# Optimization experiments

Hardware: AMD Instinct MI355X
Metric: run time of the kernel (lower is better)

Reference implementation:

```python
import jax, jax.numpy as jnp
import numpy as np

L, D, H, DH, W, G, FF = 2, 768, 12, 64, 256, 64, 3072  # W = one-sided window (attention_window=512)
B, S = 2, 4096
NEG = -1e9


def setup_inputs() -> dict:
    key = jax.random.key(0)
    ks = jax.random.split(key, 16)
    inp = {}
    inp['hidden_states'] = jax.random.normal(ks[0], (B, S, D), jnp.float32)
    # HF Longformer convention: <0 masked, >0 global, 0 local. First G tokens are global.
    inp['attention_mask'] = jnp.zeros((B, S), jnp.float32).at[:, :G].set(1.0)
    inp['padding_len'] = 0
    inp['level_hierarchy'] = 0
    def w(k, shape):
        return (jax.random.normal(k, shape, jnp.float32) * 0.02)
    for i, n in enumerate(['Wq', 'Wk', 'Wv', 'Wqg', 'Wkg', 'Wvg', 'Wo']):
        inp[n] = w(ks[1 + i], (L, D, D))
        inp['b' + n[1:].lower()] = jnp.zeros((L, D), jnp.float32)
    inp['Wi'] = w(ks[8], (L, D, FF)); inp['bi'] = jnp.zeros((L, FF), jnp.float32)
    inp['Wo2'] = w(ks[9], (L, FF, D)); inp['bo2'] = jnp.zeros((L, D), jnp.float32)
    for n in ['ln1', 'ln2']:
        inp[n + '_g'] = jnp.ones((L, D), jnp.float32)
        inp[n + '_b'] = jnp.zeros((L, D), jnp.float32)
    return inp


def _ln(x, g, b):
    mu = jnp.mean(x, -1, keepdims=True)
    var = jnp.mean(jnp.square(x - mu), -1, keepdims=True)
    return (x - mu) * jax.lax.rsqrt(var + 1e-5) * g + b


def _chunk3(x, nc, w):
    # x: [..., S, d] -> [..., nc, 3w, d]: keys of chunks (c-1, c, c+1), zero-padded at the ends
    shp = x.shape
    xr = x.reshape(shp[:-2] + (nc, w, shp[-1]))
    pad = [(0, 0)] * xr.ndim
    pad[-3] = (1, 1)
    xp = jnp.pad(xr, pad)
    return jnp.concatenate([xp[..., :-2, :, :], xp[..., 1:-1, :, :], xp[..., 2:, :, :]], axis=-2)


def _layer(h, mask, Wq, bq, Wk, bk, Wv, bv, Wqg, bqg, Wkg, bkg, Wvg, bvg,
           Wo, bo, ln1_g, ln1_b, Wi, bi, Wo2, bo2, ln2_g, ln2_b):
    Bb, Ss, Dd = h.shape
    nc = Ss // W
    scale = 1.0 / np.sqrt(DH)
    def heads(x):
        return x.reshape(Bb, Ss, H, DH).transpose(0, 2, 1, 3)  # [B,H,S,dh]
    q = heads(h @ Wq + bq) * scale
    k = heads(h @ Wk + bk)
    v = heads(h @ Wv + bv)
    # --- sliding-window (banded) attention, chunked ---
    qc = q.reshape(Bb, H, nc, W, DH)
    k3 = _chunk3(k, nc, W)  # [B,H,nc,3W,dh]
    v3 = _chunk3(v, nc, W)
    local = jnp.einsum('bhcid,bhcjd->bhcij', qc, k3)  # [B,H,nc,W,3W]
    i = jnp.arange(W)[:, None]
    j = jnp.arange(3 * W)[None, :]
    band_ok = jnp.abs(j - W - i) <= W                              # [W,3W]
    keypos = jnp.arange(nc)[:, None, None] * W + (j - W)[None]     # [nc,1,3W]
    in_range = (keypos >= 0) & (keypos < Ss)
    # masked and global keys are removed from the windowed attention (handled via global cols)
    key_local = _chunk3((mask == 0).astype(h.dtype)[..., None], nc, W)[..., 0] > 0.5  # [B,nc,3W]
    valid = band_ok[None, None] & in_range[None] & key_local[:, :, None, :]  # [B,nc,W,3W]
    local = jnp.where(valid[:, None], local, NEG)
    # --- global key columns (every token attends to the G global tokens) ---
    kg, vg = k[:, :, :G], v[:, :, :G]
    sg = jnp.einsum('bhsd,bhgd->bhsg', q, kg).reshape(Bb, H, nc, W, G)
    probs = jax.nn.softmax(jnp.concatenate([sg, local], axis=-1), axis=-1)
    pg, pl = probs[..., :G], probs[..., G:]
    out = (jnp.einsum('bhcig,bhgd->bhcid', pg, vg)
           + jnp.einsum('bhcij,bhcjd->bhcid', pl, v3)).reshape(Bb, H, Ss, DH)
    # --- global token rows: full attention with dedicated global projections ---
    qg = heads(h @ Wqg + bqg)[:, :, :G] * scale
    kgf = heads(h @ Wkg + bkg)
    vgf = heads(h @ Wvg + bvg)
    add = jnp.where(mask < 0, NEG, 0.0)[:, None, None, :]
    pgl = jax.nn.softmax(jnp.einsum('bhgd,bhsd->bhgs', qg, kgf) + add, axis=-1)
    out = out.at[:, :, :G].set(jnp.einsum('bhgs,bhsd->bhgd', pgl, vgf))
    out = jnp.where((mask < 0)[:, None, :, None], 0.0, out)
    attn = out.transpose(0, 2, 1, 3).reshape(Bb, Ss, Dd) @ Wo + bo
    h = _ln(attn + h, ln1_g, ln1_b)
    ff = jax.nn.gelu(h @ Wi + bi, approximate=False) @ Wo2 + bo2
    return _ln(ff + h, ln2_g, ln2_b)


def reference(hidden_states, attention_mask, padding_len, level_hierarchy,
              Wq, bq, Wk, bk, Wv, bv, Wqg, bqg, Wkg, bkg, Wvg, bvg,
              Wo, bo, ln1_g, ln1_b, Wi, bi, Wo2, bo2, ln2_g, ln2_b):
    h = hidden_states
    for l in range(L):
        h = _layer(h, attention_mask,
                   Wq[l], bq[l], Wk[l], bk[l], Wv[l], bv[l],
                   Wqg[l], bqg[l], Wkg[l], bkg[l], Wvg[l], bvg[l],
                   Wo[l], bo[l], ln1_g[l], ln1_b[l],
                   Wi[l], bi[l], Wo2[l], bo2[l], ln2_g[l], ln2_b[l])
    if padding_len > 0:
        h = h[:, :-padding_len]
    return h
```

## Files before the change

### kernel.cpp

```cpp
#include <hip/hip_runtime.h>

#define B_ 2
#define S_ 4096
#define D_ 768
#define H_ 12
#define DH_ 64
#define W_ 256
#define G_ 64
#define FF_ 3072
#define L_ 2
#define M_ (B_*S_)
#define NEGV -1e9f
#define NSPLIT 16

typedef short bf16x8 __attribute__((ext_vector_type(8)));
typedef float f32x4 __attribute__((ext_vector_type(4)));
typedef unsigned short u16;
typedef unsigned short u16x4 __attribute__((ext_vector_type(4)));

__device__ __forceinline__ u16 f2bf(float f) {
  union { float f; unsigned u; } a; a.f = f;
  unsigned r = a.u + 0x7FFFu + ((a.u >> 16) & 1u);
  return (u16)(r >> 16);
}
__device__ __forceinline__ float b2f(u16 u) {
  union { unsigned u; float f; } a; a.u = ((unsigned)u) << 16;
  return a.f;
}

__device__ __forceinline__ f32x4 mfma16(bf16x8 a, bf16x8 b, f32x4 c) {
  return __builtin_amdgcn_mfma_f32_16x16x32_bf16(a, b, c, 0, 0, 0);
}

__device__ __forceinline__ void gload16(const u16* g, u16* l) {
  __builtin_amdgcn_global_load_lds((const __attribute__((address_space(1))) void*)g,
                                   (__attribute__((address_space(3))) void*)l, 16, 0, 0);
}

__device__ __forceinline__ int xcd_swz(int bid, int nwg) {
  if ((nwg & 7) == 0) {
    int cpx = nwg >> 3;
    bid = (bid & 7) * cpx + (bid >> 3);
  }
  return bid;
}

struct Ptr7 { const float* p[7]; };
__global__ __launch_bounds__(256) void wtrans7(Ptr7 in, u16* __restrict__ out) {
  __shared__ float tile[32][33];
  int z = blockIdx.z;
  int slab = z >> 1, l = z & 1;
  const float* src = in.p[slab] + (size_t)l * D_ * D_;
  u16* dst = out + (size_t)z * D_ * D_;
  int k0 = blockIdx.y * 32, n0 = blockIdx.x * 32;
  int tx = threadIdx.x, ty = threadIdx.y;
#pragma unroll
  for (int i = 0; i < 4; i++)
    tile[ty + i*8][tx] = src[(size_t)(k0 + ty + i*8) * D_ + n0 + tx];
  __syncthreads();
#pragma unroll
  for (int i = 0; i < 4; i++)
    dst[(size_t)(n0 + ty + i*8) * D_ + k0 + tx] = f2bf(tile[tx][ty + i*8]);
}

__global__ __launch_bounds__(256) void wtrans(const float* __restrict__ in,
                                              u16* __restrict__ out, int K, int N) {
  __shared__ float tile[32][33];
  size_t base = (size_t)blockIdx.z * K * N;
  int k0 = blockIdx.y * 32, n0 = blockIdx.x * 32;
  int tx = threadIdx.x, ty = threadIdx.y;
#pragma unroll
  for (int i = 0; i < 4; i++)
    tile[ty + i*8][tx] = in[base + (size_t)(k0 + ty + i*8) * N + n0 + tx];
  __syncthreads();
#pragma unroll
  for (int i = 0; i < 4; i++)
    out[base + (size_t)(n0 + ty + i*8) * K + k0 + tx] = f2bf(tile[tx][ty + i*8]);
}

__global__ __launch_bounds__(256) void conv_b(const float* __restrict__ in,
                                              u16* __restrict__ outb, int n4) {
  int i = blockIdx.x * 256 + threadIdx.x;
  if (i >= n4) return;
  float4 v = ((const float4*)in)[i];
  u16x4 o;
  o[0] = f2bf(v.x); o[1] = f2bf(v.y); o[2] = f2bf(v.z); o[3] = f2bf(v.w);
  ((u16x4*)outb)[i] = o;
}

template <int MODE>
__device__ __forceinline__ float epi_post(float v) {
  if (MODE == 2) return v * 0.125f;
  if (MODE == 3) {
    float y = 0.79788456f * (v + 0.044715f * v * v * v);
    float e = __expf(fminf(2.f * y, 20.f));
    return v * e / (e + 1.f);
  }
  return v;
}

struct Bias5 { const float* p[5]; };

#define VMC4() asm volatile("s_waitcnt vmcnt(4)" ::: "memory")
#define VMC0() asm volatile("s_waitcnt vmcnt(0)" ::: "memory")
#define GPH_PRE() do { __builtin_amdgcn_s_barrier(); \
  asm volatile("s_waitcnt lgkmcnt(0)" ::: "memory"); \
  __builtin_amdgcn_sched_barrier(0); } while (0)
#define GPH_PRE_NOLDS() do { __builtin_amdgcn_s_barrier(); \
  __builtin_amdgcn_sched_barrier(0); } while (0)
#define GPH_POST() do { __builtin_amdgcn_sched_barrier(0); \
  __builtin_amdgcn_s_barrier(); } while (0)
#define GPH_MFMA(AF, BF, QM, QN) do { \
  __builtin_amdgcn_s_setprio(1); \
  _Pragma("unroll") for (int mi = 0; mi < 4; mi++) \
  _Pragma("unroll") for (int nj = 0; nj < 2; nj++) \
  _Pragma("unroll") for (int ks = 0; ks < 2; ks++) \
    acc[(QM)*4+mi][(QN)*2+nj] = mfma16(AF[mi][ks], BF[nj][ks], acc[(QM)*4+mi][(QN)*2+nj]); \
  __builtin_amdgcn_s_setprio(0); } while (0)

template <int MODE, int NW>
__global__ __launch_bounds__(512, 2) void gemm256p(const u16* __restrict__ A,
                                                   const u16* __restrict__ Wbase,
                                                   Bias5 bp,
                                                   u16* __restrict__ OutBase,
                                                   int Kdim, int Nstride, int l) {
  __shared__ u16 sA[2][16384];
  __shared__ u16 sB[2][16384];
  int gx = gridDim.x;
  int bid = blockIdx.x + blockIdx.y * gx;
  bid = xcd_swz(bid, gx * gridDim.y);
  int bxx = bid % gx, by = bid / gx;
  int bm = by * 256;
  int widx, bn;
  const u16* Bt; u16* Cb; const float* bias;
  if (NW == 5) {
    widx = bxx / 3;
    bn = (bxx % 3) * 256;
    int slab = widx + (widx >= 3 ? 1 : 0);
    Bt = Wbase + ((size_t)slab * L_ + l) * (size_t)D_ * D_;
    Cb = OutBase + (size_t)slab * M_ * D_;
    bias = bp.p[widx];
  } else {
    widx = 0;
    bn = bxx * 256;
    Bt = Wbase; Cb = OutBase; bias = bp.p[0];
  }
  int tid = threadIdx.x;
  int lane = tid & 63, wid = tid >> 6;
  int wr = wid >> 2, wc = wid & 3;
  int lr = lane & 15, lg = lane >> 4;

  int rr0 = tid >> 3, slot0 = tid & 7;
  int c80 = slot0 ^ (rr0 & 7);
  const u16* pA = A + (size_t)(bm + rr0) * Kdim + c80 * 8;
  const u16* pB = Bt + (size_t)(bn + rr0) * Kdim + c80 * 8;

  auto stA = [&](int buf, int h, int kt) {
    gload16(pA + (size_t)(h * 128) * Kdim + kt * 64, &sA[buf][(h * 1024 + tid) * 8]);
    gload16(pA + (size_t)(h * 128 + 64) * Kdim + kt * 64, &sA[buf][(h * 1024 + 512 + tid) * 8]);
  };
  auto stB = [&](int buf, int h, int kt) {
    gload16(pB + (size_t)(h * 128) * Kdim + kt * 64, &sB[buf][(h * 1024 + tid) * 8]);
    gload16(pB + (size_t)(h * 128 + 64) * Kdim + kt * 64, &sB[buf][(h * 1024 + 512 + tid) * 8]);
  };
  auto ldA = [&](bf16x8 (&af)[4][2], int c, int qm) {
#pragma unroll
    for (int mi = 0; mi < 4; mi++)
#pragma unroll
      for (int ks = 0; ks < 2; ks++) {
        int row = wr * 128 + qm * 64 + mi * 16 + lr;
        int c8 = ks * 4 + lg;
        af[mi][ks] = *(const bf16x8*)&sA[c][(row * 8 + (c8 ^ (row & 7))) * 8];
      }
  };
  auto ldB = [&](bf16x8 (&bf)[2][2], int c, int qn) {
#pragma unroll
    for (int nj = 0; nj < 2; nj++)
#pragma unroll
      for (int ks = 0; ks < 2; ks++) {
        int row = wc * 64 + qn * 32 + nj * 16 + lr;
        int c8 = ks * 4 + lg;
        bf[nj][ks] = *(const bf16x8*)&sB[c][(row * 8 + (c8 ^ (row & 7))) * 8];
      }
  };

  f32x4 acc[8][4] = {};
  int nt = Kdim >> 6;

  stA(0, 0, 0); stA(0, 1, 0);
  stB(0, 0, 0); stB(0, 1, 0);
  stB(1, 0, 1); stB(1, 1, 1);
  VMC4();
  __builtin_amdgcn_s_barrier();

  bf16x8 af[4][2], b0[2][2], b1[2][2];
  for (int kt = 0; kt < nt; kt += 2) {
    bool notlast = (kt + 2 < nt);
    ldA(af, 0, 0); ldB(b0, 0, 0);
    stA(1, 0, kt + 1);
    GPH_PRE(); GPH_MFMA(af, b0, 0, 0); GPH_POST();
    ldB(b1, 0, 1);
    stA(1, 1, kt + 1);
    GPH_PRE(); GPH_MFMA(af, b1, 0, 1); GPH_POST();
    ldA(af, 0, 1);
    if (notlast) stB(0, 0, kt + 2);
    GPH_PRE(); GPH_MFMA(af, b0, 1, 0); GPH_POST();
    if (notlast) { stB(0, 1, kt + 2); VMC4(); } else { VMC0(); }
    GPH_PRE_NOLDS(); GPH_MFMA(af, b1, 1, 1); GPH_POST();
    ldA(af, 1, 0); ldB(b0, 1, 0);
    if (notlast) stA(0, 0, kt + 2);
    GPH_PRE(); GPH_MFMA(af, b0, 0, 0); GPH_POST();
    ldB(b1, 1, 1);
    if (notlast) stA(0, 1, kt + 2);
    GPH_PRE(); GPH_MFMA(af, b1, 0, 1); GPH_POST();
    ldA(af, 1, 1);
    if (notlast) stB(1, 0, kt + 3);
    GPH_PRE(); GPH_MFMA(af, b0, 1, 0); GPH_POST();
    if (notlast) { stB(1, 1, kt + 3); VMC4(); } else { VMC0(); }
    GPH_PRE_NOLDS(); GPH_MFMA(af, b1, 1, 1); GPH_POST();
  }

  int r0 = bm + wr * 128, c0 = bn + wc * 64;
  int cr = (lane >> 4) * 4, cc = lane & 15;
  float sc = (NW == 5 && widx == 0) ? 0.125f : 1.0f;
#pragma unroll
  for (int nj = 0; nj < 4; nj++) {
    int col = c0 + nj * 16 + cc;
    float bv = bias[col];
#pragma unroll
    for (int mi = 0; mi < 8; mi++)
#pragma unroll
      for (int r = 0; r < 4; r++) {
        size_t off = (size_t)(r0 + mi * 16 + cr + r) * Nstride + col;
        Cb[off] = f2bf(epi_post<MODE>((acc[mi][nj][r] + bv) * sc));
      }
  }
}

template <int MODE>
__global__ __launch_bounds__(256) void gemm_pipe(const u16* __restrict__ A,
                                                 const u16* __restrict__ Bt,
                                                 const float* __restrict__ bias,
                                                 u16* __restrict__ Cb,
                                                 int Ndim, int Kdim, int rowTileStride) {
  __shared__ u16 sA[2][4096];
  __shared__ u16 sB[2][4096];
  int gx = gridDim.x;
  int bid = blockIdx.x + blockIdx.y * gx;
  bid = xcd_swz(bid, gx * gridDim.y);
  int bm = (bid / gx) * rowTileStride * 128;
  int bn = (bid % gx) * 128;
  int tid = threadIdx.x;
  int lane = tid & 63, w = tid >> 6;
  int r0w = (w >> 1) * 64, c0w = (w & 1) * 64;
  int lr = lane & 15, lg = lane >> 4;

  int f0 = tid, l0 = f0 >> 3, s0 = (f0 & 7) ^ (l0 & 7);
  int row0 = (l0 << 1) | (s0 >> 2), c0s = (s0 & 3) * 8;
  int f1 = tid + 256, l1 = f1 >> 3, s1 = (f1 & 7) ^ (l1 & 7);
  int row1 = (l1 << 1) | (s1 >> 2), c1s = (s1 & 3) * 8;
  const u16* A0 = A + (size_t)(bm + row0) * Kdim + c0s;
  const u16* A1 = A + (size_t)(bm + row1) * Kdim + c1s;
  const u16* B0 = Bt + (size_t)(bn + row0) * Kdim + c0s;
  const u16* B1 = Bt + (size_t)(bn + row1) * Kdim + c1s;

  int offa[4], offb[4];
#pragma unroll
  for (int i = 0; i < 4; i++) {
    int ra = r0w + i * 16 + lr;
    int la = ra >> 1, sa = ((ra & 1) << 2) | lg;
    offa[i] = la * 64 + (sa ^ (la & 7)) * 8;
    int rb = c0w + i * 16 + lr;
    int lb = rb >> 1, sb = ((rb & 1) << 2) | lg;
    offb[i] = lb * 64 + (sb ^ (lb & 7)) * 8;
  }

  int nt = Kdim >> 5;
  f32x4 acc[4][4] = {};

  gload16(A0, &sA[0][tid * 8]);
  gload16(A1, &sA[0][tid * 8 + 2048]);
  gload16(B0, &sB[0][tid * 8]);
  gload16(B1, &sB[0][tid * 8 + 2048]);

  for (int t = 0; t < nt; t++) {
    int cur = t & 1;
    if (t + 1 < nt) {
      int k1 = (t + 1) << 5;
      gload16(A0 + k1, &sA[cur ^ 1][tid * 8]);
      gload16(A1 + k1, &sA[cur ^ 1][tid * 8 + 2048]);
      gload16(B0 + k1, &sB[cur ^ 1][tid * 8]);
      gload16(B1 + k1, &sB[cur ^ 1][tid * 8 + 2048]);
      asm volatile("s_waitcnt vmcnt(4)" ::: "memory");
    } else {
      asm volatile("s_waitcnt vmcnt(0)" ::: "memory");
    }
    __builtin_amdgcn_s_barrier();
    __builtin_amdgcn_sched_barrier(0);
    bf16x8 a[4], b[4];
#pragma unroll
    for (int i = 0; i < 4; i++) a[i] = *(const bf16x8*)&sA[cur][offa[i]];
#pragma unroll
    for (int j = 0; j < 4; j++) b[j] = *(const bf16x8*)&sB[cur][offb[j]];
#pragma unroll
    for (int i = 0; i < 4; i++)
#pragma unroll
      for (int j = 0; j < 4; j++)
        acc[i][j] = mfma16(a[i], b[j], acc[i][j]);
    __builtin_amdgcn_sched_barrier(0);
    __builtin_amdgcn_s_barrier();
    __builtin_amdgcn_sched_barrier(0);
  }

  int r0 = bm + r0w, c0 = bn + c0w;
  int cr = (lane >> 4) * 4, cc = lane & 15;
#pragma unroll
  for (int j = 0; j < 4; j++) {
    int col = c0 + j * 16 + cc;
    float bv = bias[col];
#pragma unroll
    for (int i = 0; i < 4; i++)
#pragma unroll
      for (int r = 0; r < 4; r++) {
        size_t off = (size_t)(r0 + i * 16 + cr + r) * Ndim + col;
        Cb[off] = f2bf(epi_post<MODE>(acc[i][j][r] + bv));
      }
  }
}

__global__ __launch_bounds__(128) void attn_local(const u16* __restrict__ qb,
                                                  const u16* __restrict__ kb_,
                                                  const u16* __restrict__ vb,
                                                  const float* __restrict__ mask,
                                                  u16* __restrict__ ao) {
  int bid = blockIdx.x + blockIdx.y * gridDim.x;
  bid = xcd_swz(bid, 1536);
  int cx = bid & 63, bh = bid >> 6;
  int c = cx >> 2, sub = cx & 3;
  int b = bh / H_, h = bh % H_;
  int tid = threadIdx.x;
  int w = tid >> 6, lane = tid & 63;
  int lr = lane & 15, lg = lane >> 4;

  __shared__ u16 vtT[64][72];
  __shared__ u16 plds[2][32][72];
  __shared__ unsigned char vflag[576];

  int base_off = sub * 64;
  int kwin0 = c * W_ - W_;
  for (int i = tid; i < 576; i += 128) {
    int kp = kwin0 + base_off + i;
    vflag[i] = (kp >= 0 && kp < S_ && mask[b * S_ + kp] == 0.0f) ? 1 : 0;
  }

  size_t hoff = (size_t)b * S_ * D_ + h * DH_;
  int qrow0 = c * W_ + base_off + w * 32;
  bf16x8 aq[2][2];
#pragma unroll
  for (int fi = 0; fi < 2; fi++)
#pragma unroll
    for (int ks = 0; ks < 2; ks++)
      aq[fi][ks] = *(const bf16x8*)(qb + hoff + (size_t)(qrow0 + fi * 16 + lr) * D_ + ks * 32 + lg * 8);

  float ls[2][4];
  f32x4 o[2][4] = {};
#pragma unroll
  for (int fi = 0; fi < 2; fi++)
#pragma unroll
    for (int r = 0; r < 4; r++) ls[fi][r] = 0.f;

  int stg_k4 = tid >> 3, stg_j = tid & 7;
  int stg_dh0 = stg_j * 8;

  for (int kb = 0; kb <= 9; kb++) {
    int kstart = 0;
    if (kb > 0) {
      kstart = kwin0 + base_off + (kb - 1) * 64;
      if (kstart + 64 <= 0 || kstart >= S_) continue;
    }
    __syncthreads();
    {
#pragma unroll
      for (int p = 0; p < 4; p++) {
        int key = p * 16 + stg_k4;
        int kp = (kb ? kstart : 0) + key;
        bf16x8 row = *(const bf16x8*)(vb + hoff + (size_t)kp * D_ + stg_dh0);
        u16* basep = &vtT[stg_dh0][key ^ (stg_j << 3)];
#pragma unroll
        for (int e = 0; e < 8; e++) basep[e * 72] = (u16)row[e];
      }
    }
    __syncthreads();

    bf16x8 bk0[4], bk1[4];
#pragma unroll
    for (int nj = 0; nj < 4; nj++) {
      int kp = (kb ? kstart : 0) + nj * 16 + lr;
      const u16* ks8 = kb_ + hoff + (size_t)kp * D_ + lg * 8;
      bk0[nj] = *(const bf16x8*)(ks8);
      bk1[nj] = *(const bf16x8*)(ks8 + 32);
    }
    f32x4 sc[2][4];
#pragma unroll
    for (int fi = 0; fi < 2; fi++)
#pragma unroll
      for (int nj = 0; nj < 4; nj++) {
        f32x4 t = {};
        t = mfma16(aq[fi][0], bk0[nj], t);
        t = mfma16(aq[fi][1], bk1[nj], t);
        sc[fi][nj] = t;
      }

    if (kb >= 2 && kb <= 8) {
#pragma unroll
      for (int nj = 0; nj < 4; nj++) {
        bool kv = vflag[(kb - 1) * 64 + nj * 16 + lr] != 0;
#pragma unroll
        for (int fi = 0; fi < 2; fi++)
#pragma unroll
          for (int r = 0; r < 4; r++)
            sc[fi][nj][r] = kv ? sc[fi][nj][r] : NEGV;
      }
    } else if (kb > 0) {
#pragma unroll
      for (int nj = 0; nj < 4; nj++) {
        int fidx = (kb - 1) * 64 + nj * 16 + lr;
        int koff = base_off + fidx;
        bool kv = vflag[fidx] != 0;
#pragma unroll
        for (int fi = 0; fi < 2; fi++)
#pragma unroll
          for (int r = 0; r < 4; r++) {
            int wq = base_off + w * 32 + fi * 16 + lg * 4 + r;
            if (!(kv && koff >= wq && koff <= wq + 2 * W_)) sc[fi][nj][r] = NEGV;
          }
      }
    }

#pragma unroll
    for (int fi = 0; fi < 2; fi++)
#pragma unroll
      for (int r = 0; r < 4; r++) {
        float ps = 0.f;
#pragma unroll
        for (int nj = 0; nj < 4; nj++) {
          float p = __expf(sc[fi][nj][r]);
          sc[fi][nj][r] = p;
          ps += p;
        }
#pragma unroll
        for (int d = 1; d < 16; d <<= 1) ps += __shfl_xor(ps, d);
        ls[fi][r] += ps;
      }

#pragma unroll
    for (int fi = 0; fi < 2; fi++)
#pragma unroll
      for (int nj = 0; nj < 4; nj++)
#pragma unroll
        for (int r = 0; r < 4; r++)
          plds[w][fi * 16 + lg * 4 + r][nj * 16 + lr] = f2bf(sc[fi][nj][r]);
    asm volatile("s_waitcnt lgkmcnt(0)" ::: "memory");
    __builtin_amdgcn_sched_barrier(0);

    bf16x8 ap[2][2];
#pragma unroll
    for (int fi = 0; fi < 2; fi++)
#pragma unroll
      for (int ks = 0; ks < 2; ks++)
        ap[fi][ks] = *(const bf16x8*)&plds[w][fi * 16 + lr][ks * 32 + lg * 8];
#pragma unroll
    for (int dj = 0; dj < 4; dj++) {
      int xr = ((dj * 16 + lr) >> 3) & 7;
#pragma unroll
      for (int ks = 0; ks < 2; ks++) {
        bf16x8 bv = *(const bf16x8*)&vtT[dj * 16 + lr][(ks * 32 + lg * 8) ^ (xr << 3)];
        o[0][dj] = mfma16(ap[0][ks], bv, o[0][dj]);
        o[1][dj] = mfma16(ap[1][ks], bv, o[1][dj]);
      }
    }
  }

#pragma unroll
  for (int fi = 0; fi < 2; fi++)
#pragma unroll
    for (int dj = 0; dj < 4; dj++)
#pragma unroll
      for (int r = 0; r < 4; r++) {
        int row = qrow0 + fi * 16 + lg * 4 + r;
        float v = o[fi][dj][r] / ls[fi][r];
        ao[hoff + (size_t)row * D_ + dj * 16 + lr] = f2bf(v);
      }
}

__global__ __launch_bounds__(128) void attn_gsplit(const u16* __restrict__ qg,
                                                   const u16* __restrict__ kg,
                                                   const u16* __restrict__ vg,
                                                   float* __restrict__ opart,
                                                   float* __restrict__ lpart) {
  int sp = blockIdx.x, bh = blockIdx.y;
  int b = bh / H_, h = bh % H_;
  int tid = threadIdx.x, w = tid >> 6, lane = tid & 63;
  int lr = lane & 15, lg = lane >> 4;
  __shared__ u16 vtT[64][72];
  __shared__ u16 plds[2][32][72];
  size_t hoff = (size_t)b * S_ * D_ + h * DH_;
  int qrow0 = w * 32;
  bf16x8 aq[2][2];
#pragma unroll
  for (int fi = 0; fi < 2; fi++)
#pragma unroll
    for (int ks = 0; ks < 2; ks++)
      aq[fi][ks] = *(const bf16x8*)(qg + hoff + (size_t)(qrow0 + fi * 16 + lr) * D_ + ks * 32 + lg * 8);
  float ls[2][4];
  f32x4 o[2][4] = {};
#pragma unroll
  for (int fi = 0; fi < 2; fi++)
#pragma unroll
    for (int r = 0; r < 4; r++) ls[fi][r] = 0.f;

  int stg_k4 = tid >> 3, stg_j = tid & 7;
  int stg_dh0 = stg_j * 8;

  for (int kb = 0; kb < 4; kb++) {
    int kstart = sp * 256 + kb * 64;
    __syncthreads();
#pragma unroll
    for (int p = 0; p < 4; p++) {
      int key = p * 16 + stg_k4;
      bf16x8 row = *(const bf16x8*)(vg + hoff + (size_t)(kstart + key) * D_ + stg_dh0);
      u16* basep = &vtT[stg_dh0][key ^ (stg_j << 3)];
#pragma unroll
      for (int e = 0; e < 8; e++) basep[e * 72] = (u16)row[e];
    }
    __syncthreads();

    bf16x8 bk0[4], bk1[4];
#pragma unroll
    for (int nj = 0; nj < 4; nj++) {
      const u16* ks8 = kg + hoff + (size_t)(kstart + nj * 16 + lr) * D_ + lg * 8;
      bk0[nj] = *(const bf16x8*)(ks8);
      bk1[nj] = *(const bf16x8*)(ks8 + 32);
    }
    f32x4 sc[2][4];
#pragma unroll
    for (int fi = 0; fi < 2; fi++)
#pragma unroll
      for (int nj = 0; nj < 4; nj++) {
        f32x4 t = {};
        t = mfma16(aq[fi][0], bk0[nj], t);
        t = mfma16(aq[fi][1], bk1[nj], t);
        sc[fi][nj] = t;
      }
#pragma unroll
    for (int fi = 0; fi < 2; fi++)
#pragma unroll
      for (int r = 0; r < 4; r++) {
        float ps = 0.f;
#pragma unroll
        for (int nj = 0; nj < 4; nj++) {
          float p = __expf(sc[fi][nj][r]);
          sc[fi][nj][r] = p;
          ps += p;
        }
#pragma unroll
        for (int d = 1; d < 16; d <<= 1) ps += __shfl_xor(ps, d);
        ls[fi][r] += ps;
      }
#pragma unroll
    for (int fi = 0; fi < 2; fi++)
#pragma unroll
      for (int nj = 0; nj < 4; nj++)
#pragma unroll
        for (int r = 0; r < 4; r++)
          plds[w][fi * 16 + lg * 4 + r][nj * 16 + lr] = f2bf(sc[fi][nj][r]);
    asm volatile("s_waitcnt lgkmcnt(0)" ::: "memory");
    __builtin_amdgcn_sched_barrier(0);
    bf16x8 ap[2][2];
#pragma unroll
    for (int fi = 0; fi < 2; fi++)
#pragma unroll
      for (int ks = 0; ks < 2; ks++)
        ap[fi][ks] = *(const bf16x8*)&plds[w][fi * 16 + lr][ks * 32 + lg * 8];
#pragma unroll
    for (int dj = 0; dj < 4; dj++) {
      int xr = ((dj * 16 + lr) >> 3) & 7;
#pragma unroll
      for (int ks = 0; ks < 2; ks++) {
        bf16x8 bv = *(const bf16x8*)&vtT[dj * 16 + lr][(ks * 32 + lg * 8) ^ (xr << 3)];
        o[0][dj] = mfma16(ap[0][ks], bv, o[0][dj]);
        o[1][dj] = mfma16(ap[1][ks], bv, o[1][dj]);
      }
    }
  }

  size_t pbase = (size_t)(bh * NSPLIT + sp) * 64;
#pragma unroll
  for (int fi = 0; fi < 2; fi++)
#pragma unroll
    for (int r = 0; r < 4; r++) {
      int row = qrow0 + fi * 16 + lg * 4 + r;
      if (lr == 0) lpart[pbase + row] = ls[fi][r];
#pragma unroll
      for (int dj = 0; dj < 4; dj++)
        opart[(pbase + row) * 64 + dj * 16 + lr] = o[fi][dj][r];
    }
}

__global__ __launch_bounds__(256) void attn_gcombine(const float* __restrict__ opart,
                                                     const float* __restrict__ lpart,
                                                     u16* __restrict__ ao) {
  int bh = blockIdx.x;
  int b = bh / H_, h = bh % H_;
  int t = threadIdx.x;
  __shared__ float lt[64];
  if (t < 64) {
    float lsum = 0.f;
#pragma unroll
    for (int sp = 0; sp < NSPLIT; sp++)
      lsum += lpart[(size_t)(bh * NSPLIT + sp) * 64 + t];
    lt[t] = lsum;
  }
  __syncthreads();
  int row = t >> 2, c0 = (t & 3) * 16;
  float acc[16] = {};
  for (int sp = 0; sp < NSPLIT; sp++) {
    const float* op = opart + ((size_t)(bh * NSPLIT + sp) * 64 + row) * 64 + c0;
#pragma unroll
    for (int j = 0; j < 16; j++) acc[j] += op[j];
  }
  float inv = 1.f / lt[row];
  size_t hoff = (size_t)b * S_ * D_ + h * DH_;
#pragma unroll
  for (int j = 0; j < 16; j++)
    ao[hoff + (size_t)row * D_ + c0 + j] = f2bf(acc[j] * inv);
}

__global__ __launch_bounds__(192) void ln_b(const u16* __restrict__ x,
                                            const u16* __restrict__ res,
                                            const float* __restrict__ gg,
                                            const float* __restrict__ bb,
                                            u16* __restrict__ outb,
                                            float* __restrict__ outf) {
  int row = blockIdx.x, t = threadIdx.x;
  const u16* xr = x + (size_t)row * D_;
  const u16* rr = res + (size_t)row * D_;
  u16x4 xv = *(const u16x4*)&xr[t * 4];
  u16x4 rv = *(const u16x4*)&rr[t * 4];
  float v[4];
#pragma unroll
  for (int e = 0; e < 4; e++) v[e] = b2f(xv[e]) + b2f(rv[e]);
  __shared__ float sha[3], shb[3];
  float s = v[0] + v[1] + v[2] + v[3];
#pragma unroll
  for (int d = 1; d < 64; d <<= 1) s += __shfl_xor(s, d);
  if ((t & 63) == 0) sha[t >> 6] = s;
  __syncthreads();
  float mu = (sha[0] + sha[1] + sha[2]) * (1.f / 768.f);
  float dd[4], s2 = 0.f;
#pragma unroll
  for (int e = 0; e < 4; e++) { dd[e] = v[e] - mu; s2 += dd[e] * dd[e]; }
#pragma unroll
  for (int d = 1; d < 64; d <<= 1) s2 += __shfl_xor(s2, d);
  if ((t & 63) == 0) shb[t >> 6] = s2;
  __syncthreads();
  float var = (shb[0] + shb[1] + shb[2]) * (1.f / 768.f);
  float rs = rsqrtf(var + 1e-5f);
  float4 gv = *(const float4*)&gg[t * 4];
  float4 bv = *(const float4*)&bb[t * 4];
  float y0 = dd[0] * rs * gv.x + bv.x;
  float y1 = dd[1] * rs * gv.y + bv.y;
  float y2 = dd[2] * rs * gv.z + bv.z;
  float y3 = dd[3] * rs * gv.w + bv.w;
  u16x4 ov;
  ov[0] = f2bf(y0); ov[1] = f2bf(y1); ov[2] = f2bf(y2); ov[3] = f2bf(y3);
  *(u16x4*)&outb[(size_t)row * D_ + t * 4] = ov;
  if (outf) {
    float4 of = {y0, y1, y2, y3};
    *(float4*)&outf[(size_t)row * D_ + t * 4] = of;
  }
}

extern "C" void kernel_launch(void* const* d_in, const int* in_sizes, int n_in,
                              void* d_out, int out_size, void* d_ws, size_t ws_size,
                              hipStream_t stream) {
  (void)in_sizes; (void)n_in; (void)out_size; (void)ws_size;
  const float* hidden = (const float*)d_in[0];
  const float* mask   = (const float*)d_in[1];
  const float* Wq  = (const float*)d_in[4];   const float* bq  = (const float*)d_in[5];
  const float* Wk  = (const float*)d_in[6];   const float* bk  = (const float*)d_in[7];
  const float* Wv  = (const float*)d_in[8];   const float* bv  = (const float*)d_in[9];
  const float* Wqg = (const float*)d_in[10];  const float* bqg = (const float*)d_in[11];
  const float* Wkg = (const float*)d_in[12];  const float* bkg = (const float*)d_in[13];
  const float* Wvg = (const float*)d_in[14];  const float* bvg = (const float*)d_in[15];
  const float* Wo  = (const float*)d_in[16];  const float* bo  = (const float*)d_in[17];
  const float* Wi  = (const float*)d_in[18];  const float* bi  = (const float*)d_in[19];
  const float* Wo2 = (const float*)d_in[20];  const float* bo2 = (const float*)d_in[21];
  const float* ln1g = (const float*)d_in[22]; const float* ln1b = (const float*)d_in[23];
  const float* ln2g = (const float*)d_in[24]; const float* ln2b = (const float*)d_in[25];

  char* ws = (char*)d_ws;
  size_t off = 0;
  auto alloc = [&](size_t bytes) -> void* {
    void* p = ws + off;
    off += (bytes + 255) & ~(size_t)255;
    return p;
  };
  const size_t DD = (size_t)D_ * D_;
  const size_t DF = (size_t)D_ * FF_;
  u16* Wt = (u16*)alloc((7 * L_ * DD + 2 * L_ * DF) * 2);
  u16* wqg_t = Wt + 3 * L_ * DD;
  u16* wo_t  = Wt + 6 * L_ * DD;
  u16* wi_t  = Wt + 7 * L_ * DD;
  u16* wo2_t = Wt + 7 * L_ * DD + L_ * DF;

  u16* X0 = (u16*)alloc((size_t)M_ * D_ * 2);
  u16* X1 = (u16*)alloc((size_t)M_ * D_ * 2);
  u16* tb = (u16*)alloc((size_t)M_ * D_ * 2);
  u16* B_bf = (u16*)alloc((size_t)M_ * FF_ * 2);
  u16* qbf  = (u16*)alloc((size_t)M_ * D_ * 2);
  u16* kbf  = (u16*)alloc((size_t)M_ * D_ * 2);
  u16* vbf  = (u16*)alloc((size_t)M_ * D_ * 2);
  u16* qgbf = (u16*)alloc((size_t)M_ * D_ * 2);
  u16* kgbf = (u16*)alloc((size_t)M_ * D_ * 2);
  u16* vgbf = (u16*)alloc((size_t)M_ * D_ * 2);
  u16* aobf = (u16*)alloc((size_t)M_ * D_ * 2);
  float* opart = (float*)alloc((size_t)B_ * H_ * NSPLIT * 64 * 64 * 4);
  float* lpart = (float*)alloc((size_t)B_ * H_ * NSPLIT * 64 * 4);

  dim3 tb32(32, 8);
  Ptr7 wp;
  wp.p[0] = Wq; wp.p[1] = Wk; wp.p[2] = Wv; wp.p[3] = Wqg;
  wp.p[4] = Wkg; wp.p[5] = Wvg; wp.p[6] = Wo;
  wtrans7<<<dim3(24, 24, 14), tb32, 0, stream>>>(wp, Wt);
  wtrans<<<dim3(96, 24, 2), tb32, 0, stream>>>(Wi,  wi_t,  D_, FF_);
  wtrans<<<dim3(24, 96, 2), tb32, 0, stream>>>(Wo2, wo2_t, FF_, D_);

  conv_b<<<(M_ * D_ / 4 + 255) / 256, 256, 0, stream>>>(hidden, X0, M_ * D_ / 4);

  for (int l = 0; l < L_; l++) {
    size_t wdd = (size_t)l * DD;
    size_t wdf = (size_t)l * DF;
    dim3 g64(6, 64), g2(6, 2);

    Bias5 bp;
    bp.p[0] = bq  + l * D_;
    bp.p[1] = bk  + l * D_;
    bp.p[2] = bv  + l * D_;
    bp.p[3] = bkg + l * D_;
    bp.p[4] = bvg + l * D_;
    gemm256p<1, 5><<<dim3(15, 32), 512, 0, stream>>>(X0, Wt, bp, qbf, D_, D_, l);
    gemm_pipe<2><<<g2, 256, 0, stream>>>(X0, wqg_t + wdd, bqg + l * D_, qgbf, D_, D_, 32);

    attn_local<<<dim3((S_ / W_) * 4, B_ * H_), 128, 0, stream>>>(qbf, kbf, vbf, mask, aobf);
    attn_gsplit<<<dim3(NSPLIT, B_ * H_), 128, 0, stream>>>(qgbf, kgbf, vgbf, opart, lpart);
    attn_gcombine<<<B_ * H_, 256, 0, stream>>>(opart, lpart, aobf);

    gemm_pipe<1><<<g64, 256, 0, stream>>>(aobf, wo_t + wdd, bo + l * D_, tb, D_, D_, 1);
    ln_b<<<M_, 192, 0, stream>>>(tb, X0, ln1g + l * D_, ln1b + l * D_, X1, nullptr);

    Bias5 bpi; bpi.p[0] = bi + l * FF_;
    gemm256p<3, 1><<<dim3(12, 32), 512, 0, stream>>>(X1, wi_t + wdf, bpi, B_bf, D_, FF_, 0);
    gemm_pipe<1><<<g64, 256, 0, stream>>>(B_bf, wo2_t + wdf, bo2 + l * D_, tb, D_, FF_, 1);

    ln_b<<<M_, 192, 0, stream>>>(tb, X1, ln2g + l * D_, ln2b + l * D_, X0,
                                 (l == L_ - 1) ? (float*)d_out : nullptr);
  }
}
```

Baseline: 731.2 us.

## Stage GEMM epilogues through LDS for coalesced stores; triple-buffer gemm_pipe

Both GEMM kernels now write their bf16 results into a swizzled shared-memory tile first, then store full rows to global memory as 16-byte vectors. This replaces scattered 2-byte stores per accumulator element. gemm_pipe also moves from double to triple buffering of its K tiles, prefetching two stages ahead. In exchange it uses more LDS (48KB for gemm_pipe), which may lower occupancy, and adds a barrier before the store phase.

```diff
diff --git a/kernel.cpp b/kernel.cpp
--- a/kernel.cpp
+++ b/kernel.cpp
@@ -124,8 +124,7 @@
                                                    Bias5 bp,
                                                    u16* __restrict__ OutBase,
                                                    int Kdim, int Nstride, int l) {
-  __shared__ u16 sA[2][16384];
-  __shared__ u16 sB[2][16384];
+  __shared__ u16 sh[65536];
   int gx = gridDim.x;
   int bid = blockIdx.x + blockIdx.y * gx;
   bid = xcd_swz(bid, gx * gridDim.y);
@@ -156,31 +155,35 @@
   const u16* pB = Bt + (size_t)(bn + rr0) * Kdim + c80 * 8;
 
   auto stA = [&](int buf, int h, int kt) {
-    gload16(pA + (size_t)(h * 128) * Kdim + kt * 64, &sA[buf][(h * 1024 + tid) * 8]);
-    gload16(pA + (size_t)(h * 128 + 64) * Kdim + kt * 64, &sA[buf][(h * 1024 + 512 + tid) * 8]);
+    u16* base = sh + buf * 16384;
+    gload16(pA + (size_t)(h * 128) * Kdim + kt * 64, &base[(h * 1024 + tid) * 8]);
+    gload16(pA + (size_t)(h * 128 + 64) * Kdim + kt * 64, &base[(h * 1024 + 512 + tid) * 8]);
   };
   auto stB = [&](int buf, int h, int kt) {
-    gload16(pB + (size_t)(h * 128) * Kdim + kt * 64, &sB[buf][(h * 1024 + tid) * 8]);
-    gload16(pB + (size_t)(h * 128 + 64) * Kdim + kt * 64, &sB[buf][(h * 1024 + 512 + tid) * 8]);
+    u16* base = sh + 32768 + buf * 16384;
+    gload16(pB + (size_t)(h * 128) * Kdim + kt * 64, &base[(h * 1024 + tid) * 8]);
+    gload16(pB + (size_t)(h * 128 + 64) * Kdim + kt * 64, &base[(h * 1024 + 512 + tid) * 8]);
   };
   auto ldA = [&](bf16x8 (&af)[4][2], int c, int qm) {
+    const u16* base = sh + c * 16384;
 #pragma unroll
     for (int mi = 0; mi < 4; mi++)
 #pragma unroll
       for (int ks = 0; ks < 2; ks++) {
         int row = wr * 128 + qm * 64 + mi * 16 + lr;
         int c8 = ks * 4 + lg;
-        af[mi][ks] = *(const bf16x8*)&sA[c][(row * 8 + (c8 ^ (row & 7))) * 8];
+        af[mi][ks] = *(const bf16x8*)&base[(row * 8 + (c8 ^ (row & 7))) * 8];
       }
   };
   auto ldB = [&](bf16x8 (&bf)[2][2], int c, int qn) {
+    const u16* base = sh + 32768 + c * 16384;
 #pragma unroll
     for (int nj = 0; nj < 2; nj++)
 #pragma unroll
       for (int ks = 0; ks < 2; ks++) {
         int row = wc * 64 + qn * 32 + nj * 16 + lr;
         int c8 = ks * 4 + lg;
-        bf[nj][ks] = *(const bf16x8*)&sB[c][(row * 8 + (c8 ^ (row & 7))) * 8];
+        bf[nj][ks] = *(const bf16x8*)&base[(row * 8 + (c8 ^ (row & 7))) * 8];
       }
   };
 
@@ -220,20 +223,33 @@
     GPH_PRE_NOLDS(); GPH_MFMA(af, b1, 1, 1); GPH_POST();
   }
 
-  int r0 = bm + wr * 128, c0 = bn + wc * 64;
   int cr = (lane >> 4) * 4, cc = lane & 15;
-  float sc = (NW == 5 && widx == 0) ? 0.125f : 1.0f;
+  float scale = (NW == 5 && widx == 0) ? 0.125f : 1.0f;
 #pragma unroll
   for (int nj = 0; nj < 4; nj++) {
-    int col = c0 + nj * 16 + cc;
-    float bv = bias[col];
+    int col = wc * 64 + nj * 16 + cc;
+    float bv = bias[bn + col];
 #pragma unroll
     for (int mi = 0; mi < 8; mi++)
 #pragma unroll
       for (int r = 0; r < 4; r++) {
-        size_t off = (size_t)(r0 + mi * 16 + cr + r) * Nstride + col;
-        Cb[off] = f2bf(epi_post<MODE>((acc[mi][nj][r] + bv) * sc));
-      }
+        int row = wr * 128 + mi * 16 + cr + r;
+        int chunk = (col >> 3) ^ (row & 31);
+        sh[row * 256 + chunk * 8 + (col & 7)] =
+            f2bf(epi_post<MODE>((acc[mi][nj][r] + bv) * scale));
+      }
+  }
+  __syncthreads();
+  {
+    int row = tid >> 1, half = tid & 1;
+    u16* gro = Cb + (size_t)(bm + row) * Nstride + bn + half * 128;
+#pragma unroll
+    for (int c = 0; c < 16; c++) {
+      int lc = half * 16 + c;
+      int pc = lc ^ (row & 31);
+      bf16x8 v = *(const bf16x8*)&sh[row * 256 + pc * 8];
+      *(bf16x8*)(gro + c * 8) = v;
+    }
   }
 }
 
@@ -243,8 +259,7 @@
                                                  const float* __restrict__ bias,
                                                  u16* __restrict__ Cb,
                                                  int Ndim, int Kdim, int rowTileStride) {
-  __shared__ u16 sA[2][4096];
-  __shared__ u16 sB[2][4096];
+  __shared__ u16 sh[24576];
   int gx = gridDim.x;
   int bid = blockIdx.x + blockIdx.y * gx;
   bid = xcd_swz(bid, gx * gridDim.y);
@@ -275,33 +290,41 @@
     offb[i] = lb * 64 + (sb ^ (lb & 7)) * 8;
   }
 
+  auto stage = [&](int kt, int buf) {
+    int k1 = kt << 5;
+    u16* ab = sh + buf * 4096;
+    u16* bb = sh + 12288 + buf * 4096;
+    gload16(A0 + k1, &ab[tid * 8]);
+    gload16(A1 + k1, &ab[tid * 8 + 2048]);
+    gload16(B0 + k1, &bb[tid * 8]);
+    gload16(B1 + k1, &bb[tid * 8 + 2048]);
+  };
+
   int nt = Kdim >> 5;
   f32x4 acc[4][4] = {};
 
-  gload16(A0, &sA[0][tid * 8]);
-  gload16(A1, &sA[0][tid * 8 + 2048]);
-  gload16(B0, &sB[0][tid * 8]);
-  gload16(B1, &sB[0][tid * 8 + 2048]);
+  stage(0, 0);
+  if (nt > 1) stage(1, 1);
 
   for (int t = 0; t < nt; t++) {
-    int cur = t & 1;
-    if (t + 1 < nt) {
-      int k1 = (t + 1) << 5;
-      gload16(A0 + k1, &sA[cur ^ 1][tid * 8]);
-      gload16(A1 + k1, &sA[cur ^ 1][tid * 8 + 2048]);
-      gload16(B0 + k1, &sB[cur ^ 1][tid * 8]);
-      gload16(B1 + k1, &sB[cur ^ 1][tid * 8 + 2048]);
+    int cb = t % 3;
+    if (t + 2 < nt) {
+      stage(t + 2, (t + 2) % 3);
+      asm volatile("s_waitcnt vmcnt(8)" ::: "memory");
+    } else if (t + 1 < nt) {
       asm volatile("s_waitcnt vmcnt(4)" ::: "memory");
     } else {
       asm volatile("s_waitcnt vmcnt(0)" ::: "memory");
     }
     __builtin_amdgcn_s_barrier();
     __builtin_amdgcn_sched_barrier(0);
+    const u16* ab = sh + cb * 4096;
+    const u16* bb = sh + 12288 + cb * 4096;
     bf16x8 a[4], b[4];
 #pragma unroll
-    for (int i = 0; i < 4; i++) a[i] = *(const bf16x8*)&sA[cur][offa[i]];
-#pragma unroll
-    for (int j = 0; j < 4; j++) b[j] = *(const bf16x8*)&sB[cur][offb[j]];
+    for (int i = 0; i < 4; i++) a[i] = *(const bf16x8*)&ab[offa[i]];
+#pragma unroll
+    for (int j = 0; j < 4; j++) b[j] = *(const bf16x8*)&bb[offb[j]];
 #pragma unroll
     for (int i = 0; i < 4; i++)
 #pragma unroll
@@ -312,19 +335,32 @@
     __builtin_amdgcn_sched_barrier(0);
   }
 
-  int r0 = bm + r0w, c0 = bn + c0w;
   int cr = (lane >> 4) * 4, cc = lane & 15;
 #pragma unroll
   for (int j = 0; j < 4; j++) {
-    int col = c0 + j * 16 + cc;
-    float bv = bias[col];
+    int col = c0w + j * 16 + cc;
+    float bv = bias[bn + col];
 #pragma unroll
     for (int i = 0; i < 4; i++)
 #pragma unroll
       for (int r = 0; r < 4; r++) {
-        size_t off = (size_t)(r0 + i * 16 + cr + r) * Ndim + col;
-        Cb[off] = f2bf(epi_post<MODE>(acc[i][j][r] + bv));
-      }
+        int row = r0w + i * 16 + cr + r;
+        int chunk = (col >> 3) ^ (row & 15);
+        sh[row * 128 + chunk * 8 + (col & 7)] =
+            f2bf(epi_post<MODE>(acc[i][j][r] + bv));
+      }
+  }
+  __syncthreads();
+  {
+    int row = tid >> 1, half = tid & 1;
+    u16* gro = Cb + (size_t)(bm + row) * Ndim + bn + half * 64;
+#pragma unroll
+    for (int c = 0; c < 8; c++) {
+      int lc = half * 8 + c;
+      int pc = lc ^ (row & 15);
+      bf16x8 v = *(const bf16x8*)&sh[row * 128 + pc * 8];
+      *(bf16x8*)(gro + c * 8) = v;
+    }
   }
 }
 
```

Result: no change. 740.6 us (+1.3%).
